# Kernel tuning notes

Hardware: AMD Instinct MI355X
Metric: run time of the kernel (lower is better)

Reference implementation:

```python
import jax, jax.numpy as jnp
import numpy as np


def rotary_pos_emb(x):
    # x: [b, h, l, k]; interleaved rotary embedding (pairs are (0,1),(2,3),...)
    dim = x.shape[-1]
    seq = x.shape[-2]
    ts = jnp.arange(0, dim, 2, dtype=jnp.float32)
    inv_freqs = 10000.0 ** (-ts / dim)                      # [dim/2]
    grid = jnp.arange(seq, dtype=jnp.float32)[:, None] * inv_freqs[None, :]  # [l, dim/2]
    sin_embs = jnp.repeat(jnp.sin(grid), 2, axis=-1)[None]  # [1, l, dim] (interleaved repeat)
    cos_embs = jnp.repeat(jnp.cos(grid), 2, axis=-1)[None]
    x1, x2 = x[..., ::2], x[..., 1::2]
    xs = jnp.stack([-x2, x1], axis=-1).reshape(x.shape)     # interleave (-x2, x1)
    return x * cos_embs + xs * sin_embs


def setup_inputs() -> dict:
    key = jax.random.key(0)
    ks = jax.random.split(key, 5)
    b, l, d = 2, 2048, 1024
    scale = 1.0 / np.sqrt(d)
    return {
        "x": jax.random.normal(ks[0], (b, l, d), dtype=jnp.float32),
        "Wq": jax.random.normal(ks[1], (d, d), dtype=jnp.float32) * scale,
        "Wk": jax.random.normal(ks[2], (d, d), dtype=jnp.float32) * scale,
        "Wv": jax.random.normal(ks[3], (d, d), dtype=jnp.float32) * scale,
        "Wo": jax.random.normal(ks[4], (d, d), dtype=jnp.float32) * scale,
        "is_training": 0,
    }


def reference(x, Wq, Wk, Wv, Wo, is_training):
    n_heads = 16
    b, l, d = x.shape
    k_size = d // n_heads
    # NOTE: module scales q by 1/sqrt(model_size), not 1/sqrt(key_size)
    q = (x @ Wq) / jnp.sqrt(jnp.float32(d))
    q = q.reshape(b, l, n_heads, k_size).transpose(0, 2, 1, 3)  # b h l k
    k = (x @ Wk).reshape(b, l, n_heads, k_size).transpose(0, 2, 1, 3)
    v = (x @ Wv).reshape(b, l, n_heads, k_size).transpose(0, 2, 1, 3)
    q = rotary_pos_emb(q)
    k = rotary_pos_emb(k)
    logits = jnp.einsum('bhik,bhjk->bhij', q, k)  # no mask, no dropout (eval)
    a = jax.nn.softmax(logits, axis=-1)
    y = jnp.einsum('bhij,bhjv->bhiv', a, v)
    y = y.transpose(0, 2, 1, 3).reshape(b, l, d)  # b l (h v)
    return y @ Wo
```

## Files before the change

### kernel.cpp

```cpp
#include <hip/hip_runtime.h>
#include <stdint.h>

typedef unsigned short u16;
typedef unsigned int u32;
using short8 = __attribute__((ext_vector_type(8))) short;
using f32x4  = __attribute__((ext_vector_type(4))) float;
using f32x16 = __attribute__((ext_vector_type(16))) float;

typedef __attribute__((address_space(1))) unsigned int gu32;
typedef __attribute__((address_space(3))) unsigned int lu32;

__device__ __forceinline__ void gl2lds16(const u16* g, u16* lds_wave_base) {
    __builtin_amdgcn_global_load_lds(
        (gu32*)(uintptr_t)(const void*)g,
        (lu32*)(uint32_t)(uintptr_t)(void*)lds_wave_base,
        16, 0, 0);
}

__device__ inline float bf2f(u16 u) {
    union { unsigned int i; float f; } v;
    v.i = ((unsigned int)u) << 16;
    return v.f;
}
__device__ inline u16 f2bf(float f) {
    union { float f; unsigned int i; } v;
    v.f = f;
    unsigned int x = v.i;
    return (u16)((x + 0x7fffu + ((x >> 16) & 1u)) >> 16);
}
__device__ inline u32 f2bf_trunc_u32(float f) {
    union { float f; unsigned int i; } v;
    v.f = f;
    return v.i >> 16;
}

__global__ __launch_bounds__(256) void prep(
    const float* __restrict__ x, u16* __restrict__ xb,
    const float* __restrict__ w0, const float* __restrict__ w1,
    const float* __restrict__ w2, const float* __restrict__ w3,
    u16* __restrict__ t0, u16* __restrict__ t1,
    u16* __restrict__ t2, u16* __restrict__ t3,
    float2* __restrict__ tab)
{
    int tx = threadIdx.x, ty = threadIdx.y;
    int tid = ty * 32 + tx;
    int z = blockIdx.z;
    if (z == 4) {
        int bidx = blockIdx.y * 32 + blockIdx.x;
        if (bidx < 256) {
            int idx = bidx * 256 + tid;
            int pos = idx >> 5, pi = idx & 31;
            const float l2_10000_over_32 = 0.41524101186f;
            float ang = (float)pos *
                __builtin_amdgcn_exp2f(-(float)pi * l2_10000_over_32);
            float sn, cs;
            __sincosf(ang, &sn, &cs);
            tab[idx] = make_float2(cs, sn);
        }
        return;
    }
    if (z >= 5) {
        int i = (((z - 5) * 1024 + blockIdx.y * 32 + blockIdx.x) * 256 + tid) * 4;
        float4 v = *(const float4*)(x + i);
        ushort4 o;
        o.x = f2bf(v.x); o.y = f2bf(v.y); o.z = f2bf(v.z); o.w = f2bf(v.w);
        *(ushort4*)(xb + i) = o;
        return;
    }
    __shared__ u16 tile[32][33];
    const float* src; u16* dst;
    switch (z) {
        case 0:  src = w0; dst = t0; break;
        case 1:  src = w1; dst = t1; break;
        case 2:  src = w2; dst = t2; break;
        default: src = w3; dst = t3; break;
    }
    int c0 = blockIdx.x * 32, r0 = blockIdx.y * 32;
    #pragma unroll
    for (int i = 0; i < 4; i++)
        tile[ty + i * 8][tx] = f2bf(src[(size_t)(r0 + ty + i * 8) * 1024 + c0 + tx]);
    __syncthreads();
    #pragma unroll
    for (int i = 0; i < 4; i++)
        dst[(size_t)(c0 + ty + i * 8) * 1024 + r0 + tx] = tile[tx][ty + i * 8];
}

__global__ __launch_bounds__(256) void gemm_qkv(
    const u16* __restrict__ A, const u16* __restrict__ Bt,
    const float2* __restrict__ ropetab,
    u16* __restrict__ Qb, u16* __restrict__ Kb, u16* __restrict__ VT)
{
    __shared__ __align__(16) char smem[128 * 136 * 2];
    u16* As = (u16*)smem;
    u16* Bs = (u16*)(smem + 16384);

    const int tid  = threadIdx.x;
    const int lane = tid & 63;
    const int wid  = tid >> 6;
    const int quad = lane >> 4;
    const int l15  = lane & 15;
    const int wm   = wid >> 1, wn = wid & 1;

    const int m0 = blockIdx.y * 128;
    const int n0 = blockIdx.x * 128;
    const int mat = n0 >> 10;
    const int ln0 = n0 & 1023;

    f32x4 acc[4][4] = {};

    for (int k0 = 0; k0 < 1024; k0 += 64) {
        #pragma unroll
        for (int it = 0; it < 4; it++) {
            int c   = it * 256 + tid;
            int row = c >> 3;
            int col = ((c & 7) ^ (row & 7)) * 8;
            u16* lbA = &As[(size_t)(it * 256 + wid * 64) * 8];
            u16* lbB = &Bs[(size_t)(it * 256 + wid * 64) * 8];
            gl2lds16(&A [(size_t)(m0 + row) * 1024 + k0 + col], lbA);
            gl2lds16(&Bt[(size_t)(n0 + row) * 1024 + k0 + col], lbB);
        }
        __syncthreads();

        #pragma unroll
        for (int s = 0; s < 2; s++) {
            short8 a[4], b[4];
            #pragma unroll
            for (int i = 0; i < 4; i++) {
                int ra = wm * 64 + i * 16 + l15;
                int rb = wn * 64 + i * 16 + l15;
                a[i] = *(const short8*)(&As[ra * 64 + (((s * 4 + quad) ^ (ra & 7)) * 8)]);
                b[i] = *(const short8*)(&Bs[rb * 64 + (((s * 4 + quad) ^ (rb & 7)) * 8)]);
            }
            #pragma unroll
            for (int i = 0; i < 4; i++)
                #pragma unroll
                for (int j = 0; j < 4; j++)
                    acc[i][j] = __builtin_amdgcn_mfma_f32_16x16x32_bf16(a[i], b[j], acc[i][j], 0, 0, 0);
        }
        __syncthreads();
    }

    if (mat < 2) {
        u16* C = (mat == 0) ? Qb : Kb;
        const float scale = (mat == 0) ? (0.03125f * 1.44269504f) : 1.0f;
        const int odd = l15 & 1;
        #pragma unroll
        for (int i = 0; i < 4; i++)
            #pragma unroll
            for (int j = 0; j < 4; j++)
                #pragma unroll
                for (int r = 0; r < 4; r++) {
                    int lrow = wm * 64 + i * 16 + quad * 4 + r;
                    int col  = ln0 + wn * 64 + j * 16 + l15;
                    int pos  = (m0 + lrow) & 2047;
                    float v  = acc[i][j][r] * scale;
                    float vp = __shfl_xor(v, 1);
                    float2 sc = ropetab[pos * 32 + ((col & 63) >> 1)];
                    float outv = odd ? (v * sc.x + vp * sc.y)
                                     : (v * sc.x - vp * sc.y);
                    C[(size_t)(m0 + lrow) * 1024 + col] = f2bf(outv);
                }
    } else {
        u16* T = (u16*)smem;
        __syncthreads();
        #pragma unroll
        for (int i = 0; i < 4; i++)
            #pragma unroll
            for (int j = 0; j < 4; j++)
                #pragma unroll
                for (int r = 0; r < 4; r++) {
                    int lrow = wm * 64 + i * 16 + quad * 4 + r;
                    int lcol = wn * 64 + j * 16 + l15;
                    T[lcol * 136 + lrow] = f2bf(acc[i][j][r]);
                }
        __syncthreads();
        int bb2 = m0 >> 11, pos0 = m0 & 2047;
        #pragma unroll
        for (int itc = 0; itc < 8; itc++) {
            int c  = itc * 256 + tid;
            int ch = c >> 4;
            int px = (c & 15) * 8;
            int head = (ln0 + ch) >> 6;
            size_t dst = ((size_t)(bb2 * 16 + head) * 64 + (ch & 63)) * 2048
                         + pos0 + px;
            *(uint4*)(&VT[dst]) = *(const uint4*)(&T[ch * 136 + px]);
        }
    }
}

__global__ __launch_bounds__(256) void gemm_out(
    const u16* __restrict__ A, const u16* __restrict__ Bt, float* __restrict__ C)
{
    __shared__ __align__(16) u16 As[128 * 64];
    __shared__ __align__(16) u16 Bs[128 * 64];

    const int tid  = threadIdx.x;
    const int lane = tid & 63;
    const int wid  = tid >> 6;
    const int quad = lane >> 4;
    const int l15  = lane & 15;
    const int wm   = wid >> 1, wn = wid & 1;

    const int m0 = blockIdx.y * 128;
    const int n0 = blockIdx.x * 128;

    f32x4 acc[4][4] = {};

    for (int k0 = 0; k0 < 1024; k0 += 64) {
        #pragma unroll
        for (int it = 0; it < 4; it++) {
            int c   = it * 256 + tid;
            int row = c >> 3;
            int col = ((c & 7) ^ (row & 7)) * 8;
            u16* lbA = &As[(size_t)(it * 256 + wid * 64) * 8];
            u16* lbB = &Bs[(size_t)(it * 256 + wid * 64) * 8];
            gl2lds16(&A [(size_t)(m0 + row) * 1024 + k0 + col], lbA);
            gl2lds16(&Bt[(size_t)(n0 + row) * 1024 + k0 + col], lbB);
        }
        __syncthreads();

        #pragma unroll
        for (int s = 0; s < 2; s++) {
            short8 a[4], b[4];
            #pragma unroll
            for (int i = 0; i < 4; i++) {
                int ra = wm * 64 + i * 16 + l15;
                int rb = wn * 64 + i * 16 + l15;
                a[i] = *(const short8*)(&As[ra * 64 + (((s * 4 + quad) ^ (ra & 7)) * 8)]);
                b[i] = *(const short8*)(&Bs[rb * 64 + (((s * 4 + quad) ^ (rb & 7)) * 8)]);
            }
            #pragma unroll
            for (int i = 0; i < 4; i++)
                #pragma unroll
                for (int j = 0; j < 4; j++)
                    acc[i][j] = __builtin_amdgcn_mfma_f32_16x16x32_bf16(a[i], b[j], acc[i][j], 0, 0, 0);
        }
        __syncthreads();
    }

    #pragma unroll
    for (int i = 0; i < 4; i++)
        #pragma unroll
        for (int j = 0; j < 4; j++)
            #pragma unroll
            for (int r = 0; r < 4; r++) {
                int row = m0 + wm * 64 + i * 16 + quad * 4 + r;
                int col = n0 + wn * 64 + j * 16 + l15;
                C[(size_t)row * 1024 + col] = acc[i][j][r];
            }
}

__global__ __launch_bounds__(256, 2) void attn(
    const u16* __restrict__ Q, const u16* __restrict__ Kb,
    const u16* __restrict__ VT, u16* __restrict__ Y)
{
    __shared__ __align__(16) u16 Ks [128 * 64];
    __shared__ __align__(16) u16 VTs[64 * 128];
    __shared__ __align__(16) u16 Ps [4][32 * 72];

    const int tid  = threadIdx.x;
    const int lane = tid & 63, wid = tid >> 6;
    const int l31  = lane & 31, hi = lane >> 5;

    const int bh = blockIdx.x;
    const int qt = blockIdx.y;
    const int bb = bh >> 4, h = bh & 15;

    const size_t base = ((size_t)bb * 2048) * 1024 + (size_t)h * 64;

    short8 qf[4];
    {
        const u16* qp = Q + base
                      + ((size_t)qt * 128 + wid * 32 + l31) * 1024 + hi * 8;
        #pragma unroll
        for (int s = 0; s < 4; s++)
            qf[s] = *(const short8*)(qp + s * 16);
    }

    const int c0 = tid,        c1 = 256 + tid,
              c2 = 512 + tid,  c3 = 768 + tid;
    const int rk0 = c0 >> 3, ck0 = ((c0 & 7) ^ (rk0 & 7)) * 8;
    const int rk1 = c1 >> 3, ck1 = ((c1 & 7) ^ (rk1 & 7)) * 8;
    const int rk2 = c2 >> 3, ck2 = ((c2 & 7) ^ (rk2 & 7)) * 8;
    const int rk3 = c3 >> 3, ck3 = ((c3 & 7) ^ (rk3 & 7)) * 8;
    const int rv0 = c0 >> 4, cv0 = ((c0 & 15) ^ (rv0 & 15)) * 8;
    const int rv1 = c1 >> 4, cv1 = ((c1 & 15) ^ (rv1 & 15)) * 8;
    const int rv2 = c2 >> 4, cv2 = ((c2 & 15) ^ (rv2 & 15)) * 8;
    const int rv3 = c3 >> 4, cv3 = ((c3 & 15) ^ (rv3 & 15)) * 8;
    const u16* pK = Kb + base;
    const u16* pV = VT + ((size_t)bh * 64) * 2048;
    const size_t oK0 = (size_t)rk0 * 1024 + ck0, oK1 = (size_t)rk1 * 1024 + ck1;
    const size_t oK2 = (size_t)rk2 * 1024 + ck2, oK3 = (size_t)rk3 * 1024 + ck3;
    const size_t oV0 = (size_t)rv0 * 2048 + cv0, oV1 = (size_t)rv1 * 2048 + cv1;
    const size_t oV2 = (size_t)rv2 * 2048 + cv2, oV3 = (size_t)rv3 * 2048 + cv3;

    uint4 k0r, k1r, k2r, k3r, v0r, v1r, v2r, v3r;
#define LOADREGS(J0)                                                        \
    do {                                                                    \
        const size_t jk = (size_t)(J0) * 1024;                              \
        k0r = *(const uint4*)(pK + jk + oK0);                               \
        k1r = *(const uint4*)(pK + jk + oK1);                               \
        k2r = *(const uint4*)(pK + jk + oK2);                               \
        k3r = *(const uint4*)(pK + jk + oK3);                               \
        v0r = *(const uint4*)(pV + (J0) + oV0);                             \
        v1r = *(const uint4*)(pV + (J0) + oV1);                             \
        v2r = *(const uint4*)(pV + (J0) + oV2);                             \
        v3r = *(const uint4*)(pV + (J0) + oV3);                             \
    } while (0)

    f32x16 o0 = {}, o1 = {};
    float lsum = 0.0f;

    LOADREGS(0);

    for (int j0 = 0; j0 < 2048; j0 += 128) {
        __syncthreads();
        *(uint4*)(&Ks [(0 * 256 + tid) * 8]) = k0r;
        *(uint4*)(&Ks [(1 * 256 + tid) * 8]) = k1r;
        *(uint4*)(&Ks [(2 * 256 + tid) * 8]) = k2r;
        *(uint4*)(&Ks [(3 * 256 + tid) * 8]) = k3r;
        *(uint4*)(&VTs[(0 * 256 + tid) * 8]) = v0r;
        *(uint4*)(&VTs[(1 * 256 + tid) * 8]) = v1r;
        *(uint4*)(&VTs[(2 * 256 + tid) * 8]) = v2r;
        *(uint4*)(&VTs[(3 * 256 + tid) * 8]) = v3r;
        if (j0 + 128 < 2048)
            LOADREGS(j0 + 128);
        __syncthreads();

        f32x16 st[4];
        #pragma unroll
        for (int t = 0; t < 4; t++) {
            int key = t * 32 + l31;
            f32x16 z = {};
            __builtin_amdgcn_s_setprio(1);
            #pragma unroll
            for (int s = 0; s < 4; s++) {
                int chunk = ((2 * s + hi) ^ (key & 7)) * 8;
                short8 kf = *(const short8*)(&Ks[key * 64 + chunk]);
                z = __builtin_amdgcn_mfma_f32_32x32x16_bf16(kf, qf[s], z, 0, 0, 0);
            }
            __builtin_amdgcn_s_setprio(0);
            st[t] = z;
        }

        u16* ps = Ps[wid];
        #pragma unroll
        for (int hh = 0; hh < 2; hh++) {
            #pragma unroll
            for (int tt = 0; tt < 2; tt++) {
                int t = hh * 2 + tt;
                #pragma unroll
                for (int g = 0; g < 4; g++) {
                    float p0 = __builtin_amdgcn_exp2f(st[t][4 * g + 0]);
                    float p1 = __builtin_amdgcn_exp2f(st[t][4 * g + 1]);
                    float p2 = __builtin_amdgcn_exp2f(st[t][4 * g + 2]);
                    float p3 = __builtin_amdgcn_exp2f(st[t][4 * g + 3]);
                    lsum += (p0 + p1) + (p2 + p3);
                    uint2 w;
                    w.x = f2bf_trunc_u32(p0) | (f2bf_trunc_u32(p1) << 16);
                    w.y = f2bf_trunc_u32(p2) | (f2bf_trunc_u32(p3) << 16);
                    int lk = tt * 32 + g * 8 + hi * 4;
                    *(uint2*)(&ps[l31 * 72 + lk]) = w;
                }
            }
            asm volatile("s_waitcnt lgkmcnt(0)" ::: "memory");

            #pragma unroll
            for (int s = 0; s < 4; s++) {
                int koff = s * 16 + hi * 8;
                short8 pf = *(const short8*)(&ps[l31 * 72 + koff]);
                int kch = hh * 8 + 2 * s + hi;
                short8 v0 = *(const short8*)(&VTs[l31 * 128 + ((kch ^ (l31 & 15)) * 8)]);
                short8 v1 = *(const short8*)(&VTs[(32 + l31) * 128 + ((kch ^ ((32 + l31) & 15)) * 8)]);
                __builtin_amdgcn_s_setprio(1);
                o0 = __builtin_amdgcn_mfma_f32_32x32x16_bf16(pf, v0, o0, 0, 0, 0);
                o1 = __builtin_amdgcn_mfma_f32_32x32x16_bf16(pf, v1, o1, 0, 0, 0);
                __builtin_amdgcn_s_setprio(0);
            }
            asm volatile("" ::: "memory");
        }
    }
#undef LOADREGS

    lsum += __shfl_xor(lsum, 32);
    float linv = 1.0f / lsum;

    size_t qrow0 = (size_t)qt * 128 + wid * 32;
    #pragma unroll
    for (int half = 0; half < 2; half++) {
        f32x16 o = half ? o1 : o0;
        #pragma unroll
        for (int reg = 0; reg < 16; reg++) {
            int qrow = (reg & 3) + 8 * (reg >> 2) + 4 * hi;
            float nv = o[reg] * __shfl(linv, qrow);
            Y[base + (qrow0 + qrow) * 1024 + half * 32 + l31] = f2bf(nv);
        }
    }
}

extern "C" void kernel_launch(void* const* d_in, const int* in_sizes, int n_in,
                              void* d_out, int out_size, void* d_ws, size_t ws_size,
                              hipStream_t stream)
{
    const float* x  = (const float*)d_in[0];
    const float* Wq = (const float*)d_in[1];
    const float* Wk = (const float*)d_in[2];
    const float* Wv = (const float*)d_in[3];
    const float* Wo = (const float*)d_in[4];
    float* out = (float*)d_out;

    char* ws = (char*)d_ws;
    u16*    xb    = (u16*)   (ws + (0ull  << 20));
    u16*    WqkvT = (u16*)   (ws + (8ull  << 20));
    u16*    WoT   = (u16*)   (ws + (14ull << 20));
    u16*    Qb    = (u16*)   (ws + (16ull << 20));
    u16*    Kb    = (u16*)   (ws + (24ull << 20));
    u16*    VTb   = (u16*)   (ws + (32ull << 20));
    u16*    Yb    = (u16*)   (ws + (40ull << 20));
    float2* tab   = (float2*)(ws + (48ull << 20));

    prep<<<dim3(32, 32, 9), dim3(32, 8), 0, stream>>>(
        x, xb, Wq, Wk, Wv, Wo,
        WqkvT, WqkvT + (1024ull * 1024), WqkvT + (2048ull * 1024), WoT, tab);
    gemm_qkv<<<dim3(24, 32), 256, 0, stream>>>(xb, WqkvT, tab, Qb, Kb, VTb);
    attn<<<dim3(32, 16), 256, 0, stream>>>(Qb, Kb, VTb, Yb);
    gemm_out<<<dim3(8, 32), 256, 0, stream>>>(Yb, WoT, out);
}
```

Baseline: 198.0 us.

## Build P operand with cross-lane shuffles instead of LDS round trip; pad K tile

```diff
diff --git a/kernel.cpp b/kernel.cpp
--- a/kernel.cpp
+++ b/kernel.cpp
@@ -254,9 +254,8 @@
     const u16* __restrict__ Q, const u16* __restrict__ Kb,
     const u16* __restrict__ VT, u16* __restrict__ Y)
 {
-    __shared__ __align__(16) u16 Ks [128 * 64];
+    __shared__ __align__(16) u16 Ks [128 * 68];
     __shared__ __align__(16) u16 VTs[64 * 128];
-    __shared__ __align__(16) u16 Ps [4][32 * 72];
 
     const int tid  = threadIdx.x;
     const int lane = tid & 63, wid = tid >> 6;
@@ -287,6 +286,8 @@
     const int rv1 = c1 >> 4, cv1 = ((c1 & 15) ^ (rv1 & 15)) * 8;
     const int rv2 = c2 >> 4, cv2 = ((c2 & 15) ^ (rv2 & 15)) * 8;
     const int rv3 = c3 >> 4, cv3 = ((c3 & 15) ^ (rv3 & 15)) * 8;
+    const int dK0 = rk0 * 68 + (c0 & 7) * 8, dK1 = rk1 * 68 + (c1 & 7) * 8;
+    const int dK2 = rk2 * 68 + (c2 & 7) * 8, dK3 = rk3 * 68 + (c3 & 7) * 8;
     const u16* pK = Kb + base;
     const u16* pV = VT + ((size_t)bh * 64) * 2048;
     const size_t oK0 = (size_t)rk0 * 1024 + ck0, oK1 = (size_t)rk1 * 1024 + ck1;
@@ -315,10 +316,10 @@
 
     for (int j0 = 0; j0 < 2048; j0 += 128) {
         __syncthreads();
-        *(uint4*)(&Ks [(0 * 256 + tid) * 8]) = k0r;
-        *(uint4*)(&Ks [(1 * 256 + tid) * 8]) = k1r;
-        *(uint4*)(&Ks [(2 * 256 + tid) * 8]) = k2r;
-        *(uint4*)(&Ks [(3 * 256 + tid) * 8]) = k3r;
+        *(uint4*)(&Ks [dK0]) = k0r;
+        *(uint4*)(&Ks [dK1]) = k1r;
+        *(uint4*)(&Ks [dK2]) = k2r;
+        *(uint4*)(&Ks [dK3]) = k3r;
         *(uint4*)(&VTs[(0 * 256 + tid) * 8]) = v0r;
         *(uint4*)(&VTs[(1 * 256 + tid) * 8]) = v1r;
         *(uint4*)(&VTs[(2 * 256 + tid) * 8]) = v2r;
@@ -336,48 +337,49 @@
             #pragma unroll
             for (int s = 0; s < 4; s++) {
                 int chunk = ((2 * s + hi) ^ (key & 7)) * 8;
-                short8 kf = *(const short8*)(&Ks[key * 64 + chunk]);
+                short8 kf = *(const short8*)(&Ks[key * 68 + chunk]);
                 z = __builtin_amdgcn_mfma_f32_32x32x16_bf16(kf, qf[s], z, 0, 0, 0);
             }
             __builtin_amdgcn_s_setprio(0);
             st[t] = z;
         }
 
-        u16* ps = Ps[wid];
+        u32 X[4][4], Y[4][4];
+        #pragma unroll
+        for (int t = 0; t < 4; t++)
+            #pragma unroll
+            for (int g = 0; g < 4; g++) {
+                float p0 = __builtin_amdgcn_exp2f(st[t][4 * g + 0]);
+                float p1 = __builtin_amdgcn_exp2f(st[t][4 * g + 1]);
+                float p2 = __builtin_amdgcn_exp2f(st[t][4 * g + 2]);
+                float p3 = __builtin_amdgcn_exp2f(st[t][4 * g + 3]);
+                lsum += (p0 + p1) + (p2 + p3);
+                X[t][g] = f2bf_trunc_u32(p0) | (f2bf_trunc_u32(p1) << 16);
+                Y[t][g] = f2bf_trunc_u32(p2) | (f2bf_trunc_u32(p3) << 16);
+            }
+
         #pragma unroll
         for (int hh = 0; hh < 2; hh++) {
             #pragma unroll
-            for (int tt = 0; tt < 2; tt++) {
-                int t = hh * 2 + tt;
-                #pragma unroll
-                for (int g = 0; g < 4; g++) {
-                    float p0 = __builtin_amdgcn_exp2f(st[t][4 * g + 0]);
-                    float p1 = __builtin_amdgcn_exp2f(st[t][4 * g + 1]);
-                    float p2 = __builtin_amdgcn_exp2f(st[t][4 * g + 2]);
-                    float p3 = __builtin_amdgcn_exp2f(st[t][4 * g + 3]);
-                    lsum += (p0 + p1) + (p2 + p3);
-                    uint2 w;
-                    w.x = f2bf_trunc_u32(p0) | (f2bf_trunc_u32(p1) << 16);
-                    w.y = f2bf_trunc_u32(p2) | (f2bf_trunc_u32(p3) << 16);
-                    int lk = tt * 32 + g * 8 + hi * 4;
-                    *(uint2*)(&ps[l31 * 72 + lk]) = w;
-                }
-            }
-            asm volatile("s_waitcnt lgkmcnt(0)" ::: "memory");
-
-            #pragma unroll
             for (int s = 0; s < 4; s++) {
-                int koff = s * 16 + hi * 8;
-                short8 pf = *(const short8*)(&ps[l31 * 72 + koff]);
-                int kch = hh * 8 + 2 * s + hi;
+                const int t = 2 * hh + (s >> 1), u = s & 1;
+                u32 XA = X[t][2 * u], XB = X[t][2 * u + 1];
+                u32 YA = Y[t][2 * u], YB = Y[t][2 * u + 1];
+                u32 pXA = __shfl_xor(XA, 32), pXB = __shfl_xor(XB, 32);
+                u32 pYA = __shfl_xor(YA, 32), pYB = __shfl_xor(YB, 32);
+                union { u32 u4[4]; short8 s8; } pk;
+                pk.u4[0] = hi ? pXB : XA;
+                pk.u4[1] = hi ? pYB : YA;
+                pk.u4[2] = hi ? XB : pXA;
+                pk.u4[3] = hi ? YB : pYA;
+                const int kch = hh * 8 + 2 * s + hi;
                 short8 v0 = *(const short8*)(&VTs[l31 * 128 + ((kch ^ (l31 & 15)) * 8)]);
                 short8 v1 = *(const short8*)(&VTs[(32 + l31) * 128 + ((kch ^ ((32 + l31) & 15)) * 8)]);
                 __builtin_amdgcn_s_setprio(1);
-                o0 = __builtin_amdgcn_mfma_f32_32x32x16_bf16(pf, v0, o0, 0, 0, 0);
-                o1 = __builtin_amdgcn_mfma_f32_32x32x16_bf16(pf, v1, o1, 0, 0, 0);
+                o0 = __builtin_amdgcn_mfma_f32_32x32x16_bf16(pk.s8, v0, o0, 0, 0, 0);
+                o1 = __builtin_amdgcn_mfma_f32_32x32x16_bf16(pk.s8, v1, o1, 0, 0, 0);
                 __builtin_amdgcn_s_setprio(0);
             }
-            asm volatile("" ::: "memory");
         }
     }
 #undef LOADREGS
```

After: 201.2 us. About the same (+1.6%).
